# Performance work log

Hardware: AMD Instinct MI355X
Metric: run time of the kernel (lower is better)

## Reference

```python
import jax, jax.numpy as jnp
import numpy as np

B = 262144
G = 3           # n_goods
HDIM = 256
IN = G * 2 + 1  # 7


def setup_inputs() -> dict:
    key = jax.random.key(0)
    ks = jax.random.split(key, 10)
    inp = {
        "log_p": jax.random.normal(ks[0], (B, G), jnp.float32),
        "log_y": jax.random.normal(ks[1], (B, 1), jnp.float32),
        "log_xb_prev": jax.random.normal(ks[2], (B, G), jnp.float32),
        "log_q_prev": jax.random.normal(ks[3], (B, G), jnp.float32),
        # Linear weights stored torch-style: (out, in)
        "W1": jax.random.normal(ks[4], (HDIM, IN), jnp.float32) * np.sqrt(2.0 / IN),
        "b1": jnp.zeros((HDIM,), jnp.float32),
        "W2": jax.random.normal(ks[5], (HDIM, HDIM), jnp.float32) * np.sqrt(2.0 / HDIM),
        "b2": jnp.zeros((HDIM,), jnp.float32),
        "W3": jax.random.normal(ks[6], (HDIM // 2, HDIM), jnp.float32) * np.sqrt(2.0 / HDIM),
        "b3": jnp.zeros((HDIM // 2,), jnp.float32),
        "W4": jax.random.uniform(ks[7], (G, HDIM // 2), jnp.float32,
                                  minval=-0.1 * np.sqrt(6.0 / (G + HDIM // 2)),
                                  maxval=0.1 * np.sqrt(6.0 / (G + HDIM // 2))),
        "b4": jnp.zeros((G,), jnp.float32),
        "log_beta": jnp.float32(1.5),
        "log_delta": jnp.float32(np.log(0.7 / 0.3)),
    }
    return inp


def reference(log_p, log_y, log_xb_prev, log_q_prev,
              W1, b1, W2, b2, W3, b3, W4, b4, log_beta, log_delta):
    beta = jnp.clip(jnp.exp(log_beta), 0.5, 20.0)
    delta = jax.nn.sigmoid(log_delta)
    xb = delta * log_xb_prev + (1.0 - delta) * log_q_prev      # (B, G)
    x = jnp.concatenate([log_p, log_y, xb], axis=1)            # (B, 2G+1)
    h = jax.nn.silu(x @ W1.T + b1)                             # (B, 256)
    h = jax.nn.silu(h @ W2.T + b2)                             # (B, 256)
    h = jax.nn.silu(h @ W3.T + b3)                             # (B, 128)
    logits = (h @ W4.T + b4) * beta                            # (B, G)
    return jax.nn.softmax(logits, axis=1)
```

## Files before the change

kernel.cpp:

```cpp
#include <hip/hip_runtime.h>
#include <hip/hip_bf16.h>

#define B_TOTAL 262144
#define G 3
#define HD 256
#define HD2 128
#define ROWS 64
#define LDH 264

typedef short short8 __attribute__((ext_vector_type(8)));
typedef float floatx4 __attribute__((ext_vector_type(4)));

__device__ __forceinline__ unsigned short f2bf(float f) {
    unsigned u = __builtin_bit_cast(unsigned, f);
    u += 0x7FFFu + ((u >> 16) & 1u);
    return (unsigned short)(u >> 16);
}

__device__ __forceinline__ unsigned pack_bf16x2(float a, float b) {
#if __has_builtin(__builtin_amdgcn_cvt_pk_bf16_f32)
    auto r = __builtin_amdgcn_cvt_pk_bf16_f32(a, b);
    unsigned u;
    __builtin_memcpy(&u, &r, 4);
    return u;
#else
    return (unsigned)f2bf(a) | ((unsigned)f2bf(b) << 16);
#endif
}

__device__ __forceinline__ float fast_rcp(float x) {
#if __has_builtin(__builtin_amdgcn_rcpf)
    return __builtin_amdgcn_rcpf(x);
#else
    return 1.0f / x;
#endif
}
__device__ __forceinline__ float silu_f(float x) {
    return x * fast_rcp(1.0f + __expf(-x));
}

__global__ void convert_w_kernel(const float* __restrict__ W1, const float* __restrict__ W2,
                                 const float* __restrict__ W3, const float* __restrict__ W4,
                                 unsigned short* __restrict__ w1bf, unsigned short* __restrict__ w2bf,
                                 unsigned short* __restrict__ w3bf, unsigned short* __restrict__ w4bf) {
    int i = blockIdx.x * 256 + threadIdx.x;
    if (i < HD * HD)  w2bf[i] = f2bf(W2[i]);
    if (i < HD2 * HD) w3bf[i] = f2bf(W3[i]);
    if (i < HD * 32) { int r = i >> 5, k = i & 31; w1bf[i] = (k < 7) ? f2bf(W1[r * 7 + k]) : (unsigned short)0; }
    if (i < 16 * HD2) { int r = i >> 7, k = i & 127; w4bf[i] = (r < G) ? f2bf(W4[r * HD2 + k]) : (unsigned short)0; }
}

__global__ __launch_bounds__(256, 4) void mlp_kernel(
    const float* __restrict__ log_p, const float* __restrict__ log_y,
    const float* __restrict__ log_xb, const float* __restrict__ log_q,
    const float* __restrict__ b1, const float* __restrict__ b2,
    const float* __restrict__ b3, const float* __restrict__ b4,
    const float* __restrict__ p_log_beta, const float* __restrict__ p_log_delta,
    const unsigned short* __restrict__ w1bf, const unsigned short* __restrict__ w2bf,
    const unsigned short* __restrict__ w3bf, const unsigned short* __restrict__ w4bf,
    float* __restrict__ out)
{
    __shared__ __align__(16) unsigned short hA[ROWS][LDH];
    __shared__ __align__(16) unsigned short x_bf[ROWS][8];
    __shared__ __align__(16) float bias1_s[HD];
    __shared__ __align__(16) float bias2_s[HD];
    __shared__ __align__(16) float bias3_s[HD2];

    const int tid  = threadIdx.x;
    const int lane = tid & 63;
    const int wv   = tid >> 6;
    const int quad = lane >> 4;
    const int l15  = lane & 15;
    const int row0 = blockIdx.x * ROWS;

    const float beta  = fminf(fmaxf(__expf(p_log_beta[0]), 0.5f), 20.0f);
    const float delta = fast_rcp(1.0f + __expf(-p_log_delta[0]));

    bias1_s[tid] = b1[tid];
    bias2_s[tid] = b2[tid];
    if (tid < HD2) bias3_s[tid] = b3[tid];
    if (tid < ROWS) {
        const int r = row0 + tid;
        const float p0 = log_p[r * 3 + 0], p1 = log_p[r * 3 + 1], p2 = log_p[r * 3 + 2];
        const float y  = log_y[r];
        const float xb0 = delta * log_xb[r * 3 + 0] + (1.0f - delta) * log_q[r * 3 + 0];
        const float xb1 = delta * log_xb[r * 3 + 1] + (1.0f - delta) * log_q[r * 3 + 1];
        const float xb2 = delta * log_xb[r * 3 + 2] + (1.0f - delta) * log_q[r * 3 + 2];
        uint4 u0;
        u0.x = pack_bf16x2(p0, p1);
        u0.y = pack_bf16x2(p2, y);
        u0.z = pack_bf16x2(xb0, xb1);
        u0.w = pack_bf16x2(xb2, 0.0f);
        *(uint4*)&x_bf[tid][0] = u0;
    }
    __syncthreads();

    #define EPILOGUE(ACC, M, N0)                                                   \
        {                                                                          \
            const float v0 = silu_f((ACC)[0]);                                     \
            const float v1 = silu_f((ACC)[1]);                                     \
            const float v2 = silu_f((ACC)[2]);                                     \
            const float v3 = silu_f((ACC)[3]);                                     \
            uint2 u; u.x = pack_bf16x2(v0, v1); u.y = pack_bf16x2(v2, v3);         \
            *(uint2*)&hA[(M)][(N0)] = u;                                           \
        }

    {
        const int nbase = wv * 64;
        short8 aw[4], bx[4];
        #pragma unroll
        for (int nt = 0; nt < 4; ++nt)
            aw[nt] = *(const short8*)(w1bf + (nbase + nt * 16 + l15) * 32 + quad * 8);
        #pragma unroll
        for (int mt = 0; mt < 4; ++mt) {
            if (quad == 0)
                bx[mt] = *(const short8*)&x_bf[mt * 16 + l15][0];
            else
                bx[mt] = (short8){0, 0, 0, 0, 0, 0, 0, 0};
        }
        #pragma unroll
        for (int nt = 0; nt < 4; ++nt) {
            const float4 bv = *(const float4*)&bias1_s[nbase + nt * 16 + quad * 4];
            #pragma unroll
            for (int mt = 0; mt < 4; ++mt) {
                floatx4 acc = (floatx4){bv.x, bv.y, bv.z, bv.w};
                acc = __builtin_amdgcn_mfma_f32_16x16x32_bf16(aw[nt], bx[mt], acc, 0, 0, 0);
                EPILOGUE(acc, mt * 16 + l15, nbase + nt * 16 + quad * 4);
            }
        }
    }
    __syncthreads();

    {
        const int nbase = wv * 64;
        floatx4 acc[4][4];
        #pragma unroll
        for (int nt = 0; nt < 4; ++nt) {
            const float4 bv = *(const float4*)&bias2_s[nbase + nt * 16 + quad * 4];
            #pragma unroll
            for (int mt = 0; mt < 4; ++mt)
                acc[mt][nt] = (floatx4){bv.x, bv.y, bv.z, bv.w};
        }
        short8 aw[2][4];
        #pragma unroll
        for (int nt = 0; nt < 4; ++nt)
            aw[0][nt] = *(const short8*)(w2bf + (nbase + nt * 16 + l15) * HD + quad * 8);
        #pragma unroll
        for (int ks = 0; ks < 8; ++ks) {
            const int cur = ks & 1, nxt = cur ^ 1;
            if (ks < 7) {
                const int kb = (ks + 1) * 32 + quad * 8;
                #pragma unroll
                for (int nt = 0; nt < 4; ++nt)
                    aw[nxt][nt] = *(const short8*)(w2bf + (nbase + nt * 16 + l15) * HD + kb);
            }
            short8 bh[4];
            const int kb0 = ks * 32 + quad * 8;
            #pragma unroll
            for (int mt = 0; mt < 4; ++mt)
                bh[mt] = *(const short8*)&hA[mt * 16 + l15][kb0];
            #pragma unroll
            for (int mt = 0; mt < 4; ++mt)
                #pragma unroll
                for (int nt = 0; nt < 4; ++nt)
                    acc[mt][nt] = __builtin_amdgcn_mfma_f32_16x16x32_bf16(aw[cur][nt], bh[mt], acc[mt][nt], 0, 0, 0);
        }
        __syncthreads();
        #pragma unroll
        for (int mt = 0; mt < 4; ++mt) {
            #pragma unroll
            for (int nt = 0; nt < 4; ++nt)
                EPILOGUE(acc[mt][nt], mt * 16 + l15, nbase + nt * 16 + quad * 4);
        }
    }
    __syncthreads();

    {
        const int nbase = wv * 32;
        floatx4 acc[4][2];
        #pragma unroll
        for (int nt = 0; nt < 2; ++nt) {
            const float4 bv = *(const float4*)&bias3_s[nbase + nt * 16 + quad * 4];
            #pragma unroll
            for (int mt = 0; mt < 4; ++mt)
                acc[mt][nt] = (floatx4){bv.x, bv.y, bv.z, bv.w};
        }
        short8 aw[2][2];
        #pragma unroll
        for (int nt = 0; nt < 2; ++nt)
            aw[0][nt] = *(const short8*)(w3bf + (nbase + nt * 16 + l15) * HD + quad * 8);
        #pragma unroll
        for (int ks = 0; ks < 8; ++ks) {
            const int cur = ks & 1, nxt = cur ^ 1;
            if (ks < 7) {
                const int kb = (ks + 1) * 32 + quad * 8;
                #pragma unroll
                for (int nt = 0; nt < 2; ++nt)
                    aw[nxt][nt] = *(const short8*)(w3bf + (nbase + nt * 16 + l15) * HD + kb);
            }
            short8 bh[4];
            const int kb0 = ks * 32 + quad * 8;
            #pragma unroll
            for (int mt = 0; mt < 4; ++mt)
                bh[mt] = *(const short8*)&hA[mt * 16 + l15][kb0];
            #pragma unroll
            for (int mt = 0; mt < 4; ++mt)
                #pragma unroll
                for (int nt = 0; nt < 2; ++nt)
                    acc[mt][nt] = __builtin_amdgcn_mfma_f32_16x16x32_bf16(aw[cur][nt], bh[mt], acc[mt][nt], 0, 0, 0);
        }
        __syncthreads();
        #pragma unroll
        for (int mt = 0; mt < 4; ++mt) {
            #pragma unroll
            for (int nt = 0; nt < 2; ++nt)
                EPILOGUE(acc[mt][nt], mt * 16 + l15, nbase + nt * 16 + quad * 4);
        }
    }
    __syncthreads();

    {
        floatx4 acc;
        #pragma unroll
        for (int i = 0; i < 4; ++i) {
            const int rrow = quad * 4 + i;
            acc[i] = (rrow < G) ? b4[rrow] : 0.0f;
        }
        #pragma unroll
        for (int ks = 0; ks < 4; ++ks) {
            const int kb = ks * 32 + quad * 8;
            const short8 aw4 = *(const short8*)(w4bf + l15 * HD2 + kb);
            const short8 bh4 = *(const short8*)&hA[wv * 16 + l15][kb];
            acc = __builtin_amdgcn_mfma_f32_16x16x32_bf16(aw4, bh4, acc, 0, 0, 0);
        }
        if (lane < 16) {
            const float l0 = acc[0] * beta;
            const float l1 = acc[1] * beta;
            const float l2 = acc[2] * beta;
            const float m  = fmaxf(l0, fmaxf(l1, l2));
            const float e0 = __expf(l0 - m), e1 = __expf(l1 - m), e2 = __expf(l2 - m);
            const float inv = fast_rcp(e0 + e1 + e2);
            const int r = row0 + wv * 16 + l15;
            out[r * 3 + 0] = e0 * inv;
            out[r * 3 + 1] = e1 * inv;
            out[r * 3 + 2] = e2 * inv;
        }
    }
    #undef EPILOGUE
}

extern "C" void kernel_launch(void* const* d_in, const int* in_sizes, int n_in,
                              void* d_out, int out_size, void* d_ws, size_t ws_size,
                              hipStream_t stream) {
    (void)in_sizes; (void)n_in; (void)out_size; (void)ws_size;
    const float* log_p  = (const float*)d_in[0];
    const float* log_y  = (const float*)d_in[1];
    const float* log_xb = (const float*)d_in[2];
    const float* log_q  = (const float*)d_in[3];
    const float* W1 = (const float*)d_in[4];
    const float* b1 = (const float*)d_in[5];
    const float* W2 = (const float*)d_in[6];
    const float* b2 = (const float*)d_in[7];
    const float* W3 = (const float*)d_in[8];
    const float* b3 = (const float*)d_in[9];
    const float* W4 = (const float*)d_in[10];
    const float* b4 = (const float*)d_in[11];
    const float* lb = (const float*)d_in[12];
    const float* ld = (const float*)d_in[13];

    unsigned short* w2bf = (unsigned short*)d_ws;
    unsigned short* w3bf = w2bf + HD * HD;
    unsigned short* w1bf = w3bf + HD2 * HD;
    unsigned short* w4bf = w1bf + HD * 32;

    convert_w_kernel<<<256, 256, 0, stream>>>(W1, W2, W3, W4, w1bf, w2bf, w3bf, w4bf);
    mlp_kernel<<<B_TOTAL / ROWS, 256, 0, stream>>>(
        log_p, log_y, log_xb, log_q, b1, b2, b3, b4, lb, ld,
        w1bf, w2bf, w3bf, w4bf, (float*)d_out);
}
```

Measured before the change: 191.5 us.

## Double block to 128 rows and 8 waves with narrower per-wave N tiles

Each block now processes 128 rows with 512 threads, and each wave owns a narrower slice of output columns (32 for layer 2, 16 for layer 3) across all 8 M-tiles. This reuses each weight fragment over twice as many rows, roughly halving global/L2 weight traffic per row. In exchange, LDS per block doubles (about 67KB), which may cut the number of resident blocks per CU. The final layer-4 section is unchanged and its coverage of 128 rows with 8 waves is not shown.

Result: faster. 167.8 us (-12.4%).

```diff
diff --git a/kernel.cpp b/kernel.cpp
--- a/kernel.cpp
+++ b/kernel.cpp
@@ -5,7 +5,8 @@
 #define G 3
 #define HD 256
 #define HD2 128
-#define ROWS 64
+#define ROWS 128
+#define NTHREADS 512
 #define LDH 264
 
 typedef short short8 __attribute__((ext_vector_type(8)));
@@ -50,7 +51,7 @@
     if (i < 16 * HD2) { int r = i >> 7, k = i & 127; w4bf[i] = (r < G) ? f2bf(W4[r * HD2 + k]) : (unsigned short)0; }
 }
 
-__global__ __launch_bounds__(256, 4) void mlp_kernel(
+__global__ __launch_bounds__(NTHREADS, 4) void mlp_kernel(
     const float* __restrict__ log_p, const float* __restrict__ log_y,
     const float* __restrict__ log_xb, const float* __restrict__ log_q,
     const float* __restrict__ b1, const float* __restrict__ b2,
@@ -76,8 +77,7 @@
     const float beta  = fminf(fmaxf(__expf(p_log_beta[0]), 0.5f), 20.0f);
     const float delta = fast_rcp(1.0f + __expf(-p_log_delta[0]));
 
-    bias1_s[tid] = b1[tid];
-    bias2_s[tid] = b2[tid];
+    if (tid < HD) { bias1_s[tid] = b1[tid]; bias2_s[tid] = b2[tid]; }
     if (tid < HD2) bias3_s[tid] = b3[tid];
     if (tid < ROWS) {
         const int r = row0 + tid;
@@ -106,44 +106,48 @@
         }
 
     {
-        const int nbase = wv * 64;
-        short8 aw[4], bx[4];
-        #pragma unroll
-        for (int nt = 0; nt < 4; ++nt)
+        const int nbase = wv * 32;
+        short8 aw[2];
+        #pragma unroll
+        for (int nt = 0; nt < 2; ++nt)
             aw[nt] = *(const short8*)(w1bf + (nbase + nt * 16 + l15) * 32 + quad * 8);
         #pragma unroll
-        for (int mt = 0; mt < 4; ++mt) {
-            if (quad == 0)
-                bx[mt] = *(const short8*)&x_bf[mt * 16 + l15][0];
-            else
-                bx[mt] = (short8){0, 0, 0, 0, 0, 0, 0, 0};
-        }
-        #pragma unroll
-        for (int nt = 0; nt < 4; ++nt) {
-            const float4 bv = *(const float4*)&bias1_s[nbase + nt * 16 + quad * 4];
+        for (int half = 0; half < 2; ++half) {
+            short8 bx[4];
             #pragma unroll
             for (int mt = 0; mt < 4; ++mt) {
-                floatx4 acc = (floatx4){bv.x, bv.y, bv.z, bv.w};
-                acc = __builtin_amdgcn_mfma_f32_16x16x32_bf16(aw[nt], bx[mt], acc, 0, 0, 0);
-                EPILOGUE(acc, mt * 16 + l15, nbase + nt * 16 + quad * 4);
-            }
-        }
-    }
-    __syncthreads();
-
-    {
-        const int nbase = wv * 64;
-        floatx4 acc[4][4];
-        #pragma unroll
-        for (int nt = 0; nt < 4; ++nt) {
+                if (quad == 0)
+                    bx[mt] = *(const short8*)&x_bf[(half * 4 + mt) * 16 + l15][0];
+                else
+                    bx[mt] = (short8){0, 0, 0, 0, 0, 0, 0, 0};
+            }
+            #pragma unroll
+            for (int nt = 0; nt < 2; ++nt) {
+                const float4 bv = *(const float4*)&bias1_s[nbase + nt * 16 + quad * 4];
+                #pragma unroll
+                for (int mt = 0; mt < 4; ++mt) {
+                    floatx4 acc = (floatx4){bv.x, bv.y, bv.z, bv.w};
+                    acc = __builtin_amdgcn_mfma_f32_16x16x32_bf16(aw[nt], bx[mt], acc, 0, 0, 0);
+                    EPILOGUE(acc, (half * 4 + mt) * 16 + l15, nbase + nt * 16 + quad * 4);
+                }
+            }
+        }
+    }
+    __syncthreads();
+
+    {
+        const int nbase = wv * 32;
+        floatx4 acc[8][2];
+        #pragma unroll
+        for (int nt = 0; nt < 2; ++nt) {
             const float4 bv = *(const float4*)&bias2_s[nbase + nt * 16 + quad * 4];
             #pragma unroll
-            for (int mt = 0; mt < 4; ++mt)
+            for (int mt = 0; mt < 8; ++mt)
                 acc[mt][nt] = (floatx4){bv.x, bv.y, bv.z, bv.w};
         }
-        short8 aw[2][4];
-        #pragma unroll
-        for (int nt = 0; nt < 4; ++nt)
+        short8 aw[2][2];
+        #pragma unroll
+        for (int nt = 0; nt < 2; ++nt)
             aw[0][nt] = *(const short8*)(w2bf + (nbase + nt * 16 + l15) * HD + quad * 8);
         #pragma unroll
         for (int ks = 0; ks < 8; ++ks) {
@@ -151,71 +155,69 @@
             if (ks < 7) {
                 const int kb = (ks + 1) * 32 + quad * 8;
                 #pragma unroll
-                for (int nt = 0; nt < 4; ++nt)
+                for (int nt = 0; nt < 2; ++nt)
                     aw[nxt][nt] = *(const short8*)(w2bf + (nbase + nt * 16 + l15) * HD + kb);
             }
-            short8 bh[4];
             const int kb0 = ks * 32 + quad * 8;
             #pragma unroll
-            for (int mt = 0; mt < 4; ++mt)
-                bh[mt] = *(const short8*)&hA[mt * 16 + l15][kb0];
-            #pragma unroll
-            for (int mt = 0; mt < 4; ++mt)
-                #pragma unroll
-                for (int nt = 0; nt < 4; ++nt)
-                    acc[mt][nt] = __builtin_amdgcn_mfma_f32_16x16x32_bf16(aw[cur][nt], bh[mt], acc[mt][nt], 0, 0, 0);
+            for (int chunk = 0; chunk < 2; ++chunk) {
+                short8 bh[4];
+                #pragma unroll
+                for (int m = 0; m < 4; ++m)
+                    bh[m] = *(const short8*)&hA[(chunk * 4 + m) * 16 + l15][kb0];
+                #pragma unroll
+                for (int m = 0; m < 4; ++m)
+                    #pragma unroll
+                    for (int nt = 0; nt < 2; ++nt)
+                        acc[chunk * 4 + m][nt] = __builtin_amdgcn_mfma_f32_16x16x32_bf16(
+                            aw[cur][nt], bh[m], acc[chunk * 4 + m][nt], 0, 0, 0);
+            }
         }
         __syncthreads();
         #pragma unroll
-        for (int mt = 0; mt < 4; ++mt) {
-            #pragma unroll
-            for (int nt = 0; nt < 4; ++nt)
+        for (int mt = 0; mt < 8; ++mt) {
+            #pragma unroll
+            for (int nt = 0; nt < 2; ++nt)
                 EPILOGUE(acc[mt][nt], mt * 16 + l15, nbase + nt * 16 + quad * 4);
         }
     }
     __syncthreads();
 
     {
-        const int nbase = wv * 32;
-        floatx4 acc[4][2];
-        #pragma unroll
-        for (int nt = 0; nt < 2; ++nt) {
-            const float4 bv = *(const float4*)&bias3_s[nbase + nt * 16 + quad * 4];
-            #pragma unroll
-            for (int mt = 0; mt < 4; ++mt)
-                acc[mt][nt] = (floatx4){bv.x, bv.y, bv.z, bv.w};
-        }
-        short8 aw[2][2];
-        #pragma unroll
-        for (int nt = 0; nt < 2; ++nt)
-            aw[0][nt] = *(const short8*)(w3bf + (nbase + nt * 16 + l15) * HD + quad * 8);
+        const int nbase = wv * 16;
+        floatx4 acc[8];
+        {
+            const float4 bv = *(const float4*)&bias3_s[nbase + quad * 4];
+            #pragma unroll
+            for (int mt = 0; mt < 8; ++mt)
+                acc[mt] = (floatx4){bv.x, bv.y, bv.z, bv.w};
+        }
+        short8 aw[2];
+        aw[0] = *(const short8*)(w3bf + (nbase + l15) * HD + quad * 8);
         #pragma unroll
         for (int ks = 0; ks < 8; ++ks) {
             const int cur = ks & 1, nxt = cur ^ 1;
             if (ks < 7) {
                 const int kb = (ks + 1) * 32 + quad * 8;
-                #pragma unroll
-                for (int nt = 0; nt < 2; ++nt)
-                    aw[nxt][nt] = *(const short8*)(w3bf + (nbase + nt * 16 + l15) * HD + kb);
-            }
-            short8 bh[4];
+                aw[nxt] = *(const short8*)(w3bf + (nbase + l15) * HD + kb);
+            }
             const int kb0 = ks * 32 + quad * 8;
             #pragma unroll
-            for (int mt = 0; mt < 4; ++mt)
-                bh[mt] = *(const short8*)&hA[mt * 16 + l15][kb0];
-            #pragma unroll
-            for (int mt = 0; mt < 4; ++mt)
-                #pragma unroll
-                for (int nt = 0; nt < 2; ++nt)
-                    acc[mt][nt] = __builtin_amdgcn_mfma_f32_16x16x32_bf16(aw[cur][nt], bh[mt], acc[mt][nt], 0, 0, 0);
+            for (int chunk = 0; chunk < 2; ++chunk) {
+                short8 bh[4];
+                #pragma unroll
+                for (int m = 0; m < 4; ++m)
+                    bh[m] = *(const short8*)&hA[(chunk * 4 + m) * 16 + l15][kb0];
+                #pragma unroll
+                for (int m = 0; m < 4; ++m)
+                    acc[chunk * 4 + m] = __builtin_amdgcn_mfma_f32_16x16x32_bf16(
+                        aw[cur], bh[m], acc[chunk * 4 + m], 0, 0, 0);
+            }
         }
         __syncthreads();
         #pragma unroll
-        for (int mt = 0; mt < 4; ++mt) {
-            #pragma unroll
-            for (int nt = 0; nt < 2; ++nt)
-                EPILOGUE(acc[mt][nt], mt * 16 + l15, nbase + nt * 16 + quad * 4);
-        }
+        for (int mt = 0; mt < 8; ++mt)
+            EPILOGUE(acc[mt], mt * 16 + l15, nbase + quad * 4);
     }
     __syncthreads();
 
@@ -274,7 +276,7 @@
     unsigned short* w4bf = w1bf + HD * 32;
 
     convert_w_kernel<<<256, 256, 0, stream>>>(W1, W2, W3, W4, w1bf, w2bf, w3bf, w4bf);
-    mlp_kernel<<<B_TOTAL / ROWS, 256, 0, stream>>>(
+    mlp_kernel<<<B_TOTAL / ROWS, NTHREADS, 0, stream>>>(
         log_p, log_y, log_xb, log_q, b1, b2, b3, b4, lb, ld,
         w1bf, w2bf, w3bf, w4bf, (float*)d_out);
 }
```
